# Performance work log

Measured on AMD Instinct MI355X. Metric: run time of the kernel, lower is better.

The kernel has to match this reference:

```python
import jax, jax.numpy as jnp
import numpy as np
import math

B, DG, P, DA = 512, 1024, 1024, 256
LN_EPS = 1e-5  # torch LayerNorm default
EPS = 1e-12


def _ln(x, g, b):
    mu = jnp.mean(x, axis=-1, keepdims=True)
    var = jnp.mean((x - mu) ** 2, axis=-1, keepdims=True)
    return (x - mu) * jax.lax.rsqrt(var + LN_EPS) * g + b


def setup_inputs() -> dict:
    key = jax.random.key(0)
    ks = jax.random.split(key, 16)
    s = lambda fan_in: 1.0 / math.sqrt(fan_in)
    return {
        "hg": jax.random.normal(ks[0], (B, DG), jnp.float32),
        "desc_2d": jax.random.normal(ks[1], (B, P), jnp.float32),
        "Wq": jax.random.uniform(ks[2], (DA, DG), jnp.float32, -s(DG), s(DG)),
        "bq": jnp.zeros((DA,), jnp.float32),
        "wk_val": jax.random.uniform(ks[3], (DA,), jnp.float32, -1.0, 1.0),
        "bk_val": jax.random.uniform(ks[4], (DA,), jnp.float32, -1.0, 1.0),
        "wv_val": jax.random.uniform(ks[5], (DA,), jnp.float32, -1.0, 1.0),
        "bv_val": jax.random.uniform(ks[6], (DA,), jnp.float32, -1.0, 1.0),
        "Ek": jax.random.normal(ks[7], (P, DA), jnp.float32),
        "Ev": jax.random.normal(ks[8], (P, DA), jnp.float32),
        "Uq": jax.random.uniform(ks[9], (DA, DA), jnp.float32, -s(DA), s(DA)),
        "Vk": jax.random.uniform(ks[10], (DA, DA), jnp.float32, -s(DA), s(DA)),
        "ln_q_g": jnp.ones((DA,), jnp.float32), "ln_q_b": jnp.zeros((DA,), jnp.float32),
        "ln_k_g": jnp.ones((DA,), jnp.float32), "ln_k_b": jnp.zeros((DA,), jnp.float32),
        "ln_v_g": jnp.ones((DA,), jnp.float32), "ln_v_b": jnp.zeros((DA,), jnp.float32),
    }


def reference(hg, desc_2d, Wq, bq, wk_val, bk_val, wv_val, bv_val, Ek, Ev, Uq, Vk,
              ln_q_g, ln_q_b, ln_k_g, ln_k_b, ln_v_g, ln_v_b):
    # dropout is inference-mode (identity)
    q = _ln(hg @ Wq.T + bq, ln_q_g, ln_q_b)                       # (B, DA)
    # scalar -> token proj plus id embedding
    k = desc_2d[:, :, None] * wk_val + bk_val + Ek[None]          # (B, P, DA)
    v = desc_2d[:, :, None] * wv_val + bv_val + Ev[None]
    k = _ln(k, ln_k_g, ln_k_b)
    v = _ln(v, ln_v_g, ln_v_b)
    q2 = q @ Uq.T                                                 # (B, DA)
    k2 = jnp.einsum('bpd,ed->bpe', k, Vk)                         # (B, P, DA)
    e = jnp.einsum('bpd,bd->bp', k2, q2) / math.sqrt(DA)          # (B, P)
    alpha = jax.nn.sigmoid(e)
    alpha = alpha / (jnp.sum(alpha, axis=1, keepdims=True) + EPS)
    c = jnp.einsum('bp,bpd->bd', alpha, v)                        # (B, DA)
    return c, alpha
```

## Files before the change

kernel.cpp:

```cpp
#include <hip/hip_runtime.h>
#include <math.h>

#define B 512
#define DG 1024
#define P 1024
#define DA 256
#define LDP 68
#define BP (B * P)
#define BD (B * DA)

__device__ __forceinline__ float block_reduce_sum(float v, volatile float* red) {
    #pragma unroll
    for (int off = 32; off > 0; off >>= 1) v += __shfl_down(v, off, 64);
    const int lane = threadIdx.x & 63, wid = threadIdx.x >> 6;
    __syncthreads();
    if (lane == 0) red[wid] = v;
    __syncthreads();
    return red[0] + red[1] + red[2] + red[3];
}

__device__ __forceinline__ float wsum(float v) {
    #pragma unroll
    for (int m = 32; m > 0; m >>= 1) v += __shfl_xor(v, m, 64);
    return v;
}
__device__ __forceinline__ float txsum(float v) {
    #pragma unroll
    for (int m = 8; m > 0; m >>= 1) v += __shfl_xor(v, m, 16);
    return v;
}

#define FMA16(a4, b4, acc)                                   \
    acc[0][0] = fmaf(a4.x, b4.x, acc[0][0]);                 \
    acc[0][1] = fmaf(a4.x, b4.y, acc[0][1]);                 \
    acc[0][2] = fmaf(a4.x, b4.z, acc[0][2]);                 \
    acc[0][3] = fmaf(a4.x, b4.w, acc[0][3]);                 \
    acc[1][0] = fmaf(a4.y, b4.x, acc[1][0]);                 \
    acc[1][1] = fmaf(a4.y, b4.y, acc[1][1]);                 \
    acc[1][2] = fmaf(a4.y, b4.z, acc[1][2]);                 \
    acc[1][3] = fmaf(a4.y, b4.w, acc[1][3]);                 \
    acc[2][0] = fmaf(a4.z, b4.x, acc[2][0]);                 \
    acc[2][1] = fmaf(a4.z, b4.y, acc[2][1]);                 \
    acc[2][2] = fmaf(a4.z, b4.z, acc[2][2]);                 \
    acc[2][3] = fmaf(a4.z, b4.w, acc[2][3]);                 \
    acc[3][0] = fmaf(a4.w, b4.x, acc[3][0]);                 \
    acc[3][1] = fmaf(a4.w, b4.y, acc[3][1]);                 \
    acc[3][2] = fmaf(a4.w, b4.z, acc[3][2]);                 \
    acc[3][3] = fmaf(a4.w, b4.w, acc[3][3]);

#define FMA8(a0, a1, b4, acc)                                \
    acc[0][0] = fmaf(a0, b4.x, acc[0][0]);                   \
    acc[0][1] = fmaf(a0, b4.y, acc[0][1]);                   \
    acc[0][2] = fmaf(a0, b4.z, acc[0][2]);                   \
    acc[0][3] = fmaf(a0, b4.w, acc[0][3]);                   \
    acc[1][0] = fmaf(a1, b4.x, acc[1][0]);                   \
    acc[1][1] = fmaf(a1, b4.y, acc[1][1]);                   \
    acc[1][2] = fmaf(a1, b4.z, acc[1][2]);                   \
    acc[1][3] = fmaf(a1, b4.w, acc[1][3]);

__device__ __forceinline__ void stage_T(const float* __restrict__ src, int ldk, int m0, int k0,
                                        int tid, float* sD) {
    const int m = tid >> 3, k4 = (tid & 7) * 4;
    #pragma unroll
    for (int pass = 0; pass < 2; ++pass) {
        int mm = m + pass * 32;
        float4 v = *reinterpret_cast<const float4*>(&src[(m0 + mm) * ldk + k0 + k4]);
        sD[(k4 + 0) * LDP + mm] = v.x; sD[(k4 + 1) * LDP + mm] = v.y;
        sD[(k4 + 2) * LDP + mm] = v.z; sD[(k4 + 3) * LDP + mm] = v.w;
    }
}
__device__ __forceinline__ void stage_T32(const float* __restrict__ src, int ldk, int m0, int k0,
                                          int tid, float* sD) {
    const int m = tid >> 3, k4 = (tid & 7) * 4;
    float4 v = *reinterpret_cast<const float4*>(&src[(m0 + m) * ldk + k0 + k4]);
    sD[(k4 + 0) * LDP + m] = v.x; sD[(k4 + 1) * LDP + m] = v.y;
    sD[(k4 + 2) * LDP + m] = v.z; sD[(k4 + 3) * LDP + m] = v.w;
}
__device__ __forceinline__ void stage_N1(const float* __restrict__ src, int ldn, int k0, int n0,
                                         int tid, float* sD) {
    const int k = tid >> 4, n4 = (tid & 15) * 4;
    #pragma unroll
    for (int pass = 0; pass < 2; ++pass) {
        int kk = k + pass * 16;
        *reinterpret_cast<float4*>(&sD[kk * LDP + n4]) =
            *reinterpret_cast<const float4*>(&src[(k0 + kk) * ldn + n0 + n4]);
    }
}
__device__ __forceinline__ void stage_N4(const float* __restrict__ src, int pstride, int ldn,
                                         int k0, int n0, int tid, float* sD) {
    const int k = tid >> 4, n4 = (tid & 15) * 4;
    #pragma unroll
    for (int pass = 0; pass < 2; ++pass) {
        int kk = k + pass * 16;
        const float* base = &src[(k0 + kk) * ldn + n0 + n4];
        float4 v = *reinterpret_cast<const float4*>(base);
        #pragma unroll
        for (int s = 1; s < 4; ++s) {
            float4 w = *reinterpret_cast<const float4*>(base + s * pstride);
            v.x += w.x; v.y += w.y; v.z += w.z; v.w += w.w;
        }
        *reinterpret_cast<float4*>(&sD[kk * LDP + n4]) = v;
    }
}
__device__ __forceinline__ void mm_inner(const float* sA, const float* sB, int tid, float acc[4][4]) {
    const int ty4 = (tid >> 4) * 4, tx4 = (tid & 15) * 4;
    #pragma unroll
    for (int kk = 0; kk < 32; ++kk) {
        float4 a4 = *reinterpret_cast<const float4*>(&sA[kk * LDP + ty4]);
        float4 b4 = *reinterpret_cast<const float4*>(&sB[kk * LDP + tx4]);
        FMA16(a4, b4, acc)
    }
}

__global__ __launch_bounds__(256) void KA(const float* __restrict__ hg, const float* __restrict__ Wq,
                                          const float* __restrict__ Uq, const float* __restrict__ Vk,
                                          const float* __restrict__ Ek, const float* __restrict__ Ev,
                                          const float* __restrict__ wk, const float* __restrict__ bk,
                                          const float* __restrict__ wv, const float* __restrict__ bv,
                                          const float* __restrict__ gk, const float* __restrict__ bkln,
                                          float* __restrict__ qp, float* __restrict__ Gp,
                                          float* __restrict__ UqT, float* __restrict__ Sacc,
                                          float* __restrict__ pst, float* __restrict__ scal4,
                                          float* __restrict__ vec4) {
    __shared__ __align__(16) float sA[32 * LDP];
    __shared__ __align__(16) float sB[32 * LDP];
    const int tid = threadIdx.x;
    const int t = blockIdx.x;
    const int ty4 = (tid >> 4) * 4, tx4 = (tid & 15) * 4;

    if (t < 256) {
        const int mt = t & 7, nt = (t >> 3) & 3, ks = t >> 5;
        const int b0 = mt * 64, d0 = nt * 64, kc = ks * 128;
        float acc[4][4] = {};
        for (int kt = 0; kt < 128; kt += 32) {
            stage_T(hg, DG, b0, kc + kt, tid, sA);
            stage_T(Wq, DG, d0, kc + kt, tid, sB);
            __syncthreads();
            mm_inner(sA, sB, tid, acc);
            __syncthreads();
        }
        float* outp = qp + ks * BD;
        #pragma unroll
        for (int i = 0; i < 4; ++i) {
            float4 o = make_float4(acc[i][0], acc[i][1], acc[i][2], acc[i][3]);
            *reinterpret_cast<float4*>(&outp[(b0 + ty4 + i) * DA + d0 + tx4]) = o;
        }
    } else if (t < 512) {
        const int t2 = t - 256;
        const int et = t2 & 3, pt = (t2 >> 2) & 15, ks = t2 >> 6;
        const int e0 = et * 64, p0 = pt * 64, kc = ks * 64;
        float acc[4][4] = {};
        for (int kt = 0; kt < 64; kt += 32) {
            const int kg = kc + kt;
            {
                const int m = tid >> 3, k4 = (tid & 7) * 4;
                float4 g = *reinterpret_cast<const float4*>(&gk[kg + k4]);
                #pragma unroll
                for (int pass = 0; pass < 2; ++pass) {
                    int mm = m + pass * 32;
                    float4 v = *reinterpret_cast<const float4*>(&Vk[(e0 + mm) * DA + kg + k4]);
                    sA[(k4 + 0) * LDP + mm] = v.x * g.x; sA[(k4 + 1) * LDP + mm] = v.y * g.y;
                    sA[(k4 + 2) * LDP + mm] = v.z * g.z; sA[(k4 + 3) * LDP + mm] = v.w * g.w;
                }
            }
            stage_T(Ek, DA, p0, kg, tid, sB);
            __syncthreads();
            mm_inner(sA, sB, tid, acc);
            __syncthreads();
        }
        float* outp = Gp + ks * (DA * P);
        #pragma unroll
        for (int i = 0; i < 4; ++i) {
            float4 o = make_float4(acc[i][0], acc[i][1], acc[i][2], acc[i][3]);
            *reinterpret_cast<float4*>(&outp[(e0 + ty4 + i) * P + p0 + tx4]) = o;
        }
    } else if (t < 576) {
        const int b2 = t - 512;
        const int e0 = (b2 & 7) * 32, f0 = (b2 >> 3) * 32;
        const int col = tid & 31, row8 = tid >> 5;
        #pragma unroll
        for (int pass = 0; pass < 4; ++pass) {
            int r = row8 + pass * 8;
            sA[r * 33 + col] = Uq[(e0 + r) * DA + f0 + col];
        }
        __syncthreads();
        #pragma unroll
        for (int pass = 0; pass < 4; ++pass) {
            int r = row8 + pass * 8;
            UqT[(f0 + r) * DA + e0 + col] = sA[col * 33 + r];
        }
    } else if (t == 576) {
        #pragma unroll
        for (int j = 0; j < 8; ++j) Sacc[j * 256 + tid] = 0.f;
        float* w4  = sA;
        float* tmp = sB;
        float gkd = gk[tid];
        w4[0 * 256 + tid] = wk[tid] * gkd;
        w4[1 * 256 + tid] = bk[tid] * gkd;
        w4[2 * 256 + tid] = gkd;
        w4[3 * 256 + tid] = bkln[tid];
        __syncthreads();
        const int dl = tid & 15, eg = tid >> 4;
        for (int eb = 0; eb < 16; ++eb) {
            int e = eb * 16 + eg;
            float p0 = 0.f, p1 = 0.f, p2 = 0.f, p3 = 0.f;
            #pragma unroll
            for (int tt = 0; tt < 16; ++tt) {
                int d = dl + tt * 16;
                float v = Vk[e * DA + d];
                p0 = fmaf(v, w4[d], p0);
                p1 = fmaf(v, w4[256 + d], p1);
                p2 = fmaf(v, w4[512 + d], p2);
                p3 = fmaf(v, w4[768 + d], p3);
            }
            #pragma unroll
            for (int m = 8; m > 0; m >>= 1) {
                p0 += __shfl_xor(p0, m, 16);
                p1 += __shfl_xor(p1, m, 16);
                p2 += __shfl_xor(p2, m, 16);
                p3 += __shfl_xor(p3, m, 16);
            }
            if (dl == 0) {
                tmp[e * 4 + 0] = p0; tmp[e * 4 + 1] = p1;
                tmp[e * 4 + 2] = p2; tmp[e * 4 + 3] = p3;
            }
        }
        __syncthreads();
        float a0 = 0.f, a1 = 0.f, a2 = 0.f, a3 = 0.f;
        for (int e = 0; e < 256; ++e) {
            float u = Uq[e * DA + tid];
            a0 = fmaf(u, tmp[e * 4 + 0], a0);
            a1 = fmaf(u, tmp[e * 4 + 1], a1);
            a2 = fmaf(u, tmp[e * 4 + 2], a2);
            a3 = fmaf(u, tmp[e * 4 + 3], a3);
        }
        vec4[tid] = a0; vec4[256 + tid] = a1; vec4[512 + tid] = a2; vec4[768 + tid] = a3;
    } else {
        const int tp = t - 577;
        const int wid = tid >> 6, lane = tid & 63;
        const int p = tp * 4 + wid;
        const int d4 = lane * 4;
        const float inv = 1.0f / DA;
        float4 ek4 = *reinterpret_cast<const float4*>(&Ek[p * DA + d4]);
        float4 ev4 = *reinterpret_cast<const float4*>(&Ev[p * DA + d4]);
        float4 wk4 = *reinterpret_cast<const float4*>(&wk[d4]);
        float4 bk4 = *reinterpret_cast<const float4*>(&bk[d4]);
        float4 wv4 = *reinterpret_cast<const float4*>(&wv[d4]);
        float4 bv4 = *reinterpret_cast<const float4*>(&bv[d4]);
        float ck0 = bk4.x + ek4.x, ck1 = bk4.y + ek4.y, ck2 = bk4.z + ek4.z, ck3 = bk4.w + ek4.w;
        float cv0 = bv4.x + ev4.x, cv1 = bv4.y + ev4.y, cv2 = bv4.z + ev4.z, cv3 = bv4.w + ev4.w;
        float Sck  = wsum(ck0 + ck1 + ck2 + ck3);
        float Sck2 = wsum(ck0*ck0 + ck1*ck1 + ck2*ck2 + ck3*ck3);
        float Swck = wsum(wk4.x*ck0 + wk4.y*ck1 + wk4.z*ck2 + wk4.w*ck3);
        float Scv  = wsum(cv0 + cv1 + cv2 + cv3);
        float Scv2 = wsum(cv0*cv0 + cv1*cv1 + cv2*cv2 + cv3*cv3);
        float Swcv = wsum(wv4.x*cv0 + wv4.y*cv1 + wv4.z*cv2 + wv4.w*cv3);
        float Swk  = wsum(wk4.x + wk4.y + wk4.z + wk4.w);
        float Swv  = wsum(wv4.x + wv4.y + wv4.z + wv4.w);
        float mwk = Swk * inv, mwv = Swv * inv;
        float mck = Sck * inv, mcv = Scv * inv;
        if (lane == 0) {
            pst[0 * P + p] = mck;
            pst[1 * P + p] = Swck * inv - mwk * mck;
            pst[2 * P + p] = Sck2 * inv - mck * mck;
            pst[3 * P + p] = mcv;
            pst[4 * P + p] = Swcv * inv - mwv * mcv;
            pst[5 * P + p] = Scv2 * inv - mcv * mcv;
        }
        if (p == 0) {
            float Swk2 = wsum(wk4.x*wk4.x + wk4.y*wk4.y + wk4.z*wk4.z + wk4.w*wk4.w);
            float Swv2 = wsum(wv4.x*wv4.x + wv4.y*wv4.y + wv4.z*wv4.z + wv4.w*wv4.w);
            if (lane == 0) {
                scal4[0] = mwk;
                scal4[1] = Swk2 * inv - mwk * mwk;
                scal4[2] = mwv;
                scal4[3] = Swv2 * inv - mwv * mwv;
            }
        }
    }
}

__global__ __launch_bounds__(256) void KC(const float* __restrict__ qp, const float* __restrict__ bq,
                                          const float* __restrict__ gq, const float* __restrict__ bqln,
                                          const float* __restrict__ vec4, const float* __restrict__ UqT,
                                          float* __restrict__ q2out, float* __restrict__ bscal) {
    __shared__ __align__(16) float q_lds[DA];
    __shared__ float red[4];
    const int b = blockIdx.x, d = threadIdx.x;
    float x = bq[d];
    #pragma unroll
    for (int ks = 0; ks < 8; ++ks) x += qp[ks * BD + b * DA + d];
    float mu = block_reduce_sum(x, red) * (1.0f / DA);
    float xc = x - mu;
    float var = block_reduce_sum(xc * xc, red) * (1.0f / DA);
    float qv = xc * rsqrtf(var + 1e-5f) * gq[d] + bqln[d];
    q_lds[d] = qv;
    float Wg = block_reduce_sum(qv * vec4[d], red);
    float Cg = block_reduce_sum(qv * vec4[256 + d], red);
    float G_ = block_reduce_sum(qv * vec4[512 + d], red);
    float Bb = block_reduce_sum(qv * vec4[768 + d], red);
    if (d == 0) {
        bscal[b] = Wg; bscal[B + b] = Cg;
        bscal[2 * B + b] = G_; bscal[3 * B + b] = Bb;
    }
    float q2 = 0.f;
    for (int f = 0; f < DA; f += 4) {
        float4 qf = *reinterpret_cast<const float4*>(&q_lds[f]);
        q2 = fmaf(qf.x, UqT[(f + 0) * DA + d], q2);
        q2 = fmaf(qf.y, UqT[(f + 1) * DA + d], q2);
        q2 = fmaf(qf.z, UqT[(f + 2) * DA + d], q2);
        q2 = fmaf(qf.w, UqT[(f + 3) * DA + d], q2);
    }
    q2out[b * DA + d] = q2;
}

__global__ __launch_bounds__(256) void KD(const float* __restrict__ q2, const float* __restrict__ Gp,
                                          const float* __restrict__ desc, const float* __restrict__ bscal,
                                          const float* __restrict__ pst, const float* __restrict__ scal4,
                                          float* __restrict__ ubuf, float* __restrict__ wbuf,
                                          float* __restrict__ Sacc) {
    __shared__ __align__(16) float sA[32 * LDP];
    __shared__ __align__(16) float sB[32 * LDP];
    const int tid = threadIdx.x, t = blockIdx.x;
    const int tx = tid & 15, ty = tid >> 4;
    const int tx4 = tx * 4;
    const int b0 = (t & 15) * 32, p0 = (t >> 4) * 64;
    float acc[2][4] = {};
    for (int kt = 0; kt < 256; kt += 32) {
        stage_T32(q2, DA, b0, kt, tid, sA);
        stage_N4(Gp, DA * P, P, kt, p0, tid, sB);
        __syncthreads();
        #pragma unroll
        for (int kk = 0; kk < 32; ++kk) {
            float a0 = sA[kk * LDP + ty * 2 + 0];
            float a1 = sA[kk * LDP + ty * 2 + 1];
            float4 b4 = *reinterpret_cast<const float4*>(&sB[kk * LDP + tx4]);
            FMA8(a0, a1, b4, acc)
        }
        __syncthreads();
    }
    const float mwk = scal4[0], Ak = scal4[1], mwv = scal4[2], Av = scal4[3];
    #pragma unroll
    for (int i = 0; i < 2; ++i) {
        const int b = b0 + ty * 2 + i;
        const float Wg = bscal[b], Cg = bscal[B + b], G_ = bscal[2 * B + b], Bb = bscal[3 * B + b];
        float4 uo, wo;
        float* up = &uo.x; float* wp = &wo.x;
        float us = 0.f, ws_ = 0.f, wss = 0.f, wms = 0.f;
        #pragma unroll
        for (int j = 0; j < 4; ++j) {
            const int p = p0 + tx4 + j;
            float s = desc[b * P + p];
            float mck = pst[p], Bk = pst[P + p], Ck = pst[2 * P + p];
            float var = fmaf(s, fmaf(s, Ak, 2.0f * Bk), Ck);
            float rstd = rsqrtf(var + 1e-5f);
            float mu = fmaf(s, mwk, mck);
            float e = (rstd * (fmaf(s, Wg, Cg) + acc[i][j] - mu * G_) + Bb) * 0.0625f;
            float uu = 1.0f / (1.0f + expf(-e));
            float mcv = pst[3 * P + p], Bv = pst[4 * P + p], Cv = pst[5 * P + p];
            float varv = fmaf(s, fmaf(s, Av, 2.0f * Bv), Cv);
            float rv = rsqrtf(varv + 1e-5f);
            float ww = uu * rv;
            up[j] = uu; wp[j] = ww;
            us += uu; ws_ += ww;
            wss = fmaf(ww, s, wss);
            wms = fmaf(ww, fmaf(s, mwv, mcv), wms);
        }
        *reinterpret_cast<float4*>(&ubuf[b * P + p0 + tx4]) = uo;
        *reinterpret_cast<float4*>(&wbuf[b * P + p0 + tx4]) = wo;
        us = txsum(us); ws_ = txsum(ws_); wss = txsum(wss); wms = txsum(wms);
        if (tx == 0) {
            atomicAdd(&Sacc[b], us);
            atomicAdd(&Sacc[B + b], ws_);
            atomicAdd(&Sacc[2 * B + b], wss);
            atomicAdd(&Sacc[3 * B + b], wms);
        }
    }
}

__global__ __launch_bounds__(256) void KF(const float* __restrict__ wbuf, const float* __restrict__ Ev,
                                          float* __restrict__ cpart) {
    __shared__ __align__(16) float sA[32 * LDP];
    __shared__ __align__(16) float sB[32 * LDP];
    const int tid = threadIdx.x, t = blockIdx.x;
    const int ty4 = (tid >> 4) * 4, tx4 = (tid & 15) * 4;
    const int mt = t & 7, nt = (t >> 3) & 3, ks = t >> 5;
    const int b0 = mt * 64, d0 = nt * 64, kc = ks * 128;
    float acc[4][4] = {};
    for (int kt = 0; kt < 128; kt += 32) {
        stage_T(wbuf, P, b0, kc + kt, tid, sA);
        stage_N1(Ev, DA, kc + kt, d0, tid, sB);
        __syncthreads();
        mm_inner(sA, sB, tid, acc);
        __syncthreads();
    }
    float* outp = cpart + ks * BD;
    #pragma unroll
    for (int i = 0; i < 4; ++i) {
        float4 o = make_float4(acc[i][0], acc[i][1], acc[i][2], acc[i][3]);
        *reinterpret_cast<float4*>(&outp[(b0 + ty4 + i) * DA + d0 + tx4]) = o;
    }
}

__global__ __launch_bounds__(256) void KG(const float* __restrict__ cpart, const float* __restrict__ Sacc,
                                          const float* __restrict__ ubuf,
                                          const float* __restrict__ gv, const float* __restrict__ wv,
                                          const float* __restrict__ bvv, const float* __restrict__ bvln,
                                          float* __restrict__ alpha_out, float* __restrict__ out_c) {
    const int b = blockIdx.x, tid = threadIdx.x;
    const float S = Sacc[b], SB = Sacc[B + b], SBs = Sacc[2 * B + b], SBm = Sacc[3 * B + b];
    const float invS = 1.0f / (S + 1e-12f);
    const float T = S * invS;
    #pragma unroll
    for (int j = 0; j < 4; ++j) {
        int p = j * 256 + tid;
        alpha_out[b * P + p] = ubuf[b * P + p] * invS;
    }
    const int d = tid;
    float csum = 0.f;
    #pragma unroll
    for (int ks = 0; ks < 8; ++ks) csum += cpart[ks * BD + b * DA + d];
    out_c[b * DA + d] =
        invS * (gv[d] * (wv[d] * SBs + bvv[d] * SB + csum - SBm)) + bvln[d] * T;
}

extern "C" void kernel_launch(void* const* d_in, const int* in_sizes, int n_in,
                              void* d_out, int out_size, void* d_ws, size_t ws_size,
                              hipStream_t stream) {
    (void)in_sizes; (void)n_in; (void)out_size; (void)ws_size;
    const float* hg   = (const float*)d_in[0];
    const float* desc = (const float*)d_in[1];
    const float* Wq   = (const float*)d_in[2];
    const float* bq   = (const float*)d_in[3];
    const float* wk   = (const float*)d_in[4];
    const float* bk   = (const float*)d_in[5];
    const float* wv   = (const float*)d_in[6];
    const float* bv   = (const float*)d_in[7];
    const float* Ek   = (const float*)d_in[8];
    const float* Ev   = (const float*)d_in[9];
    const float* Uq   = (const float*)d_in[10];
    const float* Vk   = (const float*)d_in[11];
    const float* gq   = (const float*)d_in[12];
    const float* bqln = (const float*)d_in[13];
    const float* gk   = (const float*)d_in[14];
    const float* bkln = (const float*)d_in[15];
    const float* gv   = (const float*)d_in[16];
    const float* bvln = (const float*)d_in[17];

    float* out = (float*)d_out;
    float* out_c = out;
    float* out_alpha = out + BD;

    float* ws = (float*)d_ws;
    float* qp    = ws;
    float* Gp    = ws + 1048576;
    float* UqT   = ws + 2097152;
    float* q2    = ws + 2162688;
    float* ubuf  = ws + 2293760;
    float* wbuf  = ws + 2818048;
    float* cpart = ws + 3342336;
    float* vec4  = ws + 4390912;
    float* bscal = ws + 4391936;
    float* Sacc  = ws + 4393984;
    float* pst   = ws + 4396032;
    float* scal4 = ws + 4402176;

    KA<<<833, 256, 0, stream>>>(hg, Wq, Uq, Vk, Ek, Ev, wk, bk, wv, bv, gk, bkln,
                                qp, Gp, UqT, Sacc, pst, scal4, vec4);
    KC<<<512, 256, 0, stream>>>(qp, bq, gq, bqln, vec4, UqT, q2, bscal);
    KD<<<256, 256, 0, stream>>>(q2, Gp, desc, bscal, pst, scal4, ubuf, wbuf, Sacc);
    KF<<<256, 256, 0, stream>>>(wbuf, Ev, cpart);
    KG<<<512, 256, 0, stream>>>(cpart, Sacc, ubuf, gv, wv, bv, bvln, out_alpha, out_c);
}
```

Baseline: 70.31 us.

## Fuse five kernels into one persistent kernel with grid-wide atomic barriers

Replaces the five separate kernel launches with one persistent 256-block kernel. Each former kernel becomes a phase that loops over its tiles, and phases are separated by a software grid barrier built on atomic counters that a memset clears before launch. The Vk·Ek split-K factor also drops from 4 to 2 partials, so the score stage sums fewer slices of Gp. This removes launch gaps and the tail between kernels, but it depends on all 256 blocks being co-resident. It also has to run many phases with fewer blocks than the original grids (833 and 512 tiles).

```diff
diff --git a/kernel.cpp b/kernel.cpp
--- a/kernel.cpp
+++ b/kernel.cpp
@@ -8,6 +8,7 @@
 #define LDP 68
 #define BP (B * P)
 #define BD (B * DA)
+#define NBLK 256
 
 __device__ __forceinline__ float block_reduce_sum(float v, volatile float* red) {
     #pragma unroll
@@ -18,7 +19,6 @@
     __syncthreads();
     return red[0] + red[1] + red[2] + red[3];
 }
-
 __device__ __forceinline__ float wsum(float v) {
     #pragma unroll
     for (int m = 32; m > 0; m >>= 1) v += __shfl_xor(v, m, 64);
@@ -86,7 +86,7 @@
             *reinterpret_cast<const float4*>(&src[(k0 + kk) * ldn + n0 + n4]);
     }
 }
-__device__ __forceinline__ void stage_N4(const float* __restrict__ src, int pstride, int ldn,
+__device__ __forceinline__ void stage_N2(const float* __restrict__ src, int pstride, int ldn,
                                          int k0, int n0, int tid, float* sD) {
     const int k = tid >> 4, n4 = (tid & 15) * 4;
     #pragma unroll
@@ -94,11 +94,8 @@
         int kk = k + pass * 16;
         const float* base = &src[(k0 + kk) * ldn + n0 + n4];
         float4 v = *reinterpret_cast<const float4*>(base);
-        #pragma unroll
-        for (int s = 1; s < 4; ++s) {
-            float4 w = *reinterpret_cast<const float4*>(base + s * pstride);
-            v.x += w.x; v.y += w.y; v.z += w.z; v.w += w.w;
-        }
+        float4 w = *reinterpret_cast<const float4*>(base + pstride);
+        v.x += w.x; v.y += w.y; v.z += w.z; v.w += w.w;
         *reinterpret_cast<float4*>(&sD[kk * LDP + n4]) = v;
     }
 }
@@ -112,363 +109,360 @@
     }
 }
 
-__global__ __launch_bounds__(256) void KA(const float* __restrict__ hg, const float* __restrict__ Wq,
-                                          const float* __restrict__ Uq, const float* __restrict__ Vk,
-                                          const float* __restrict__ Ek, const float* __restrict__ Ev,
-                                          const float* __restrict__ wk, const float* __restrict__ bk,
-                                          const float* __restrict__ wv, const float* __restrict__ bv,
-                                          const float* __restrict__ gk, const float* __restrict__ bkln,
-                                          float* __restrict__ qp, float* __restrict__ Gp,
-                                          float* __restrict__ UqT, float* __restrict__ Sacc,
-                                          float* __restrict__ pst, float* __restrict__ scal4,
-                                          float* __restrict__ vec4) {
+__device__ __forceinline__ void gbar(unsigned* cnt, int ph) {
+    __syncthreads();
+    if (threadIdx.x == 0) {
+        __threadfence();
+        atomicAdd(&cnt[ph], 1u);
+        while (atomicAdd(&cnt[ph], 0u) < (unsigned)NBLK) {
+            __builtin_amdgcn_s_sleep(2);
+        }
+        __threadfence();
+    }
+    __syncthreads();
+}
+
+struct KArgs {
+    const float *hg, *desc, *Wq, *bq, *wk, *bk, *wv, *bv, *Ek, *Ev, *Uq, *Vk;
+    const float *gq, *bqln, *gk, *bkln, *gv, *bvln;
+    float *out_c, *out_alpha;
+    float *Sacc; unsigned* cnt;
+    float *qp, *Gp, *UqT, *q2, *ubuf, *wbuf, *cpart, *vec4, *bscal, *pst, *scal4;
+};
+
+__global__ __launch_bounds__(256) void mega(KArgs A) {
     __shared__ __align__(16) float sA[32 * LDP];
     __shared__ __align__(16) float sB[32 * LDP];
-    const int tid = threadIdx.x;
-    const int t = blockIdx.x;
+    __shared__ float red[4];
+    const int tid = threadIdx.x, bid = blockIdx.x;
     const int ty4 = (tid >> 4) * 4, tx4 = (tid & 15) * 4;
 
-    if (t < 256) {
+    for (int t = bid; t < 705; t += NBLK) {
+        if (t < 256) {
+            const int mt = t & 7, nt = (t >> 3) & 3, ks = t >> 5;
+            const int b0 = mt * 64, d0 = nt * 64, kc = ks * 128;
+            float acc[4][4] = {};
+            for (int kt = 0; kt < 128; kt += 32) {
+                stage_T(A.hg, DG, b0, kc + kt, tid, sA);
+                stage_T(A.Wq, DG, d0, kc + kt, tid, sB);
+                __syncthreads();
+                mm_inner(sA, sB, tid, acc);
+                __syncthreads();
+            }
+            float* outp = A.qp + ks * BD;
+            #pragma unroll
+            for (int i = 0; i < 4; ++i) {
+                float4 o = make_float4(acc[i][0], acc[i][1], acc[i][2], acc[i][3]);
+                *reinterpret_cast<float4*>(&outp[(b0 + ty4 + i) * DA + d0 + tx4]) = o;
+            }
+        } else if (t < 384) {
+            const int t2 = t - 256;
+            const int et = t2 & 3, pt = (t2 >> 2) & 15, ks = t2 >> 6;
+            const int e0 = et * 64, p0 = pt * 64, kc = ks * 128;
+            float acc[4][4] = {};
+            for (int kt = 0; kt < 128; kt += 32) {
+                const int kg = kc + kt;
+                {
+                    const int m = tid >> 3, k4 = (tid & 7) * 4;
+                    float4 g = *reinterpret_cast<const float4*>(&A.gk[kg + k4]);
+                    #pragma unroll
+                    for (int pass = 0; pass < 2; ++pass) {
+                        int mm = m + pass * 32;
+                        float4 v = *reinterpret_cast<const float4*>(&A.Vk[(e0 + mm) * DA + kg + k4]);
+                        sA[(k4 + 0) * LDP + mm] = v.x * g.x; sA[(k4 + 1) * LDP + mm] = v.y * g.y;
+                        sA[(k4 + 2) * LDP + mm] = v.z * g.z; sA[(k4 + 3) * LDP + mm] = v.w * g.w;
+                    }
+                }
+                stage_T(A.Ek, DA, p0, kg, tid, sB);
+                __syncthreads();
+                mm_inner(sA, sB, tid, acc);
+                __syncthreads();
+            }
+            float* outp = A.Gp + ks * (DA * P);
+            #pragma unroll
+            for (int i = 0; i < 4; ++i) {
+                float4 o = make_float4(acc[i][0], acc[i][1], acc[i][2], acc[i][3]);
+                *reinterpret_cast<float4*>(&outp[(e0 + ty4 + i) * P + p0 + tx4]) = o;
+            }
+        } else if (t < 448) {
+            const int b2 = t - 384;
+            const int e0 = (b2 & 7) * 32, f0 = (b2 >> 3) * 32;
+            const int col = tid & 31, row8 = tid >> 5;
+            #pragma unroll
+            for (int pass = 0; pass < 4; ++pass) {
+                int r = row8 + pass * 8;
+                sA[r * 33 + col] = A.Uq[(e0 + r) * DA + f0 + col];
+            }
+            __syncthreads();
+            #pragma unroll
+            for (int pass = 0; pass < 4; ++pass) {
+                int r = row8 + pass * 8;
+                A.UqT[(f0 + r) * DA + e0 + col] = sA[col * 33 + r];
+            }
+        } else if (t == 448) {
+            float* w4  = sA;
+            float* tmp = sB;
+            float gkd = A.gk[tid];
+            w4[0 * 256 + tid] = A.wk[tid] * gkd;
+            w4[1 * 256 + tid] = A.bk[tid] * gkd;
+            w4[2 * 256 + tid] = gkd;
+            w4[3 * 256 + tid] = A.bkln[tid];
+            __syncthreads();
+            const int dl = tid & 15, eg = tid >> 4;
+            for (int eb = 0; eb < 16; ++eb) {
+                int e = eb * 16 + eg;
+                float p0 = 0.f, p1 = 0.f, p2 = 0.f, p3 = 0.f;
+                #pragma unroll
+                for (int tt = 0; tt < 16; ++tt) {
+                    int d = dl + tt * 16;
+                    float v = A.Vk[e * DA + d];
+                    p0 = fmaf(v, w4[d], p0);
+                    p1 = fmaf(v, w4[256 + d], p1);
+                    p2 = fmaf(v, w4[512 + d], p2);
+                    p3 = fmaf(v, w4[768 + d], p3);
+                }
+                #pragma unroll
+                for (int m = 8; m > 0; m >>= 1) {
+                    p0 += __shfl_xor(p0, m, 16);
+                    p1 += __shfl_xor(p1, m, 16);
+                    p2 += __shfl_xor(p2, m, 16);
+                    p3 += __shfl_xor(p3, m, 16);
+                }
+                if (dl == 0) {
+                    tmp[e * 4 + 0] = p0; tmp[e * 4 + 1] = p1;
+                    tmp[e * 4 + 2] = p2; tmp[e * 4 + 3] = p3;
+                }
+            }
+            __syncthreads();
+            float a0 = 0.f, a1 = 0.f, a2 = 0.f, a3 = 0.f;
+            for (int e = 0; e < 256; ++e) {
+                float u = A.Uq[e * DA + tid];
+                a0 = fmaf(u, tmp[e * 4 + 0], a0);
+                a1 = fmaf(u, tmp[e * 4 + 1], a1);
+                a2 = fmaf(u, tmp[e * 4 + 2], a2);
+                a3 = fmaf(u, tmp[e * 4 + 3], a3);
+            }
+            A.vec4[tid] = a0; A.vec4[256 + tid] = a1;
+            A.vec4[512 + tid] = a2; A.vec4[768 + tid] = a3;
+        } else {
+            const int tp = t - 449;
+            const int wid = tid >> 6, lane = tid & 63;
+            const int p = tp * 4 + wid;
+            const int d4 = lane * 4;
+            const float inv = 1.0f / DA;
+            float4 ek4 = *reinterpret_cast<const float4*>(&A.Ek[p * DA + d4]);
+            float4 ev4 = *reinterpret_cast<const float4*>(&A.Ev[p * DA + d4]);
+            float4 wk4 = *reinterpret_cast<const float4*>(&A.wk[d4]);
+            float4 bk4 = *reinterpret_cast<const float4*>(&A.bk[d4]);
+            float4 wv4 = *reinterpret_cast<const float4*>(&A.wv[d4]);
+            float4 bv4 = *reinterpret_cast<const float4*>(&A.bv[d4]);
+            float ck0 = bk4.x + ek4.x, ck1 = bk4.y + ek4.y, ck2 = bk4.z + ek4.z, ck3 = bk4.w + ek4.w;
+            float cv0 = bv4.x + ev4.x, cv1 = bv4.y + ev4.y, cv2 = bv4.z + ev4.z, cv3 = bv4.w + ev4.w;
+            float Sck  = wsum(ck0 + ck1 + ck2 + ck3);
+            float Sck2 = wsum(ck0*ck0 + ck1*ck1 + ck2*ck2 + ck3*ck3);
+            float Swck = wsum(wk4.x*ck0 + wk4.y*ck1 + wk4.z*ck2 + wk4.w*ck3);
+            float Scv  = wsum(cv0 + cv1 + cv2 + cv3);
+            float Scv2 = wsum(cv0*cv0 + cv1*cv1 + cv2*cv2 + cv3*cv3);
+            float Swcv = wsum(wv4.x*cv0 + wv4.y*cv1 + wv4.z*cv2 + wv4.w*cv3);
+            float Swk  = wsum(wk4.x + wk4.y + wk4.z + wk4.w);
+            float Swv  = wsum(wv4.x + wv4.y + wv4.z + wv4.w);
+            float mwk = Swk * inv, mwv = Swv * inv;
+            float mck = Sck * inv, mcv = Scv * inv;
+            if (lane == 0) {
+                A.pst[0 * P + p] = mck;
+                A.pst[1 * P + p] = Swck * inv - mwk * mck;
+                A.pst[2 * P + p] = Sck2 * inv - mck * mck;
+                A.pst[3 * P + p] = mcv;
+                A.pst[4 * P + p] = Swcv * inv - mwv * mcv;
+                A.pst[5 * P + p] = Scv2 * inv - mcv * mcv;
+            }
+            if (p == 0) {
+                float Swk2 = wsum(wk4.x*wk4.x + wk4.y*wk4.y + wk4.z*wk4.z + wk4.w*wk4.w);
+                float Swv2 = wsum(wv4.x*wv4.x + wv4.y*wv4.y + wv4.z*wv4.z + wv4.w*wv4.w);
+                if (lane == 0) {
+                    A.scal4[0] = mwk;
+                    A.scal4[1] = Swk2 * inv - mwk * mwk;
+                    A.scal4[2] = mwv;
+                    A.scal4[3] = Swv2 * inv - mwv * mwv;
+                }
+            }
+        }
+        __syncthreads();
+    }
+    gbar(A.cnt, 0);
+
+    for (int t = bid; t < 512; t += NBLK) {
+        const int b = t, d = tid;
+        float* q_lds = sA;
+        float x = A.bq[d];
+        #pragma unroll
+        for (int ks = 0; ks < 8; ++ks) x += A.qp[ks * BD + b * DA + d];
+        float mu = block_reduce_sum(x, red) * (1.0f / DA);
+        float xc = x - mu;
+        float var = block_reduce_sum(xc * xc, red) * (1.0f / DA);
+        float qv = xc * rsqrtf(var + 1e-5f) * A.gq[d] + A.bqln[d];
+        q_lds[d] = qv;
+        float Wg = block_reduce_sum(qv * A.vec4[d], red);
+        float Cg = block_reduce_sum(qv * A.vec4[256 + d], red);
+        float G_ = block_reduce_sum(qv * A.vec4[512 + d], red);
+        float Bb = block_reduce_sum(qv * A.vec4[768 + d], red);
+        if (d == 0) {
+            A.bscal[b] = Wg; A.bscal[B + b] = Cg;
+            A.bscal[2 * B + b] = G_; A.bscal[3 * B + b] = Bb;
+        }
+        float q2 = 0.f;
+        for (int f = 0; f < DA; f += 4) {
+            float4 qf = *reinterpret_cast<const float4*>(&q_lds[f]);
+            q2 = fmaf(qf.x, A.UqT[(f + 0) * DA + d], q2);
+            q2 = fmaf(qf.y, A.UqT[(f + 1) * DA + d], q2);
+            q2 = fmaf(qf.z, A.UqT[(f + 2) * DA + d], q2);
+            q2 = fmaf(qf.w, A.UqT[(f + 3) * DA + d], q2);
+        }
+        A.q2[b * DA + d] = q2;
+        __syncthreads();
+    }
+    gbar(A.cnt, 1);
+
+    for (int t = bid; t < 256; t += NBLK) {
+        const int tx = tid & 15, ty = tid >> 4;
+        const int b0 = (t & 15) * 32, p0 = (t >> 4) * 64;
+        float acc[2][4] = {};
+        for (int kt = 0; kt < 256; kt += 32) {
+            stage_T32(A.q2, DA, b0, kt, tid, sA);
+            stage_N2(A.Gp, DA * P, P, kt, p0, tid, sB);
+            __syncthreads();
+            #pragma unroll
+            for (int kk = 0; kk < 32; ++kk) {
+                float a0 = sA[kk * LDP + ty * 2 + 0];
+                float a1 = sA[kk * LDP + ty * 2 + 1];
+                float4 b4 = *reinterpret_cast<const float4*>(&sB[kk * LDP + tx4]);
+                FMA8(a0, a1, b4, acc)
+            }
+            __syncthreads();
+        }
+        const float mwk = A.scal4[0], Ak = A.scal4[1], mwv = A.scal4[2], Av = A.scal4[3];
+        #pragma unroll
+        for (int i = 0; i < 2; ++i) {
+            const int b = b0 + ty * 2 + i;
+            const float Wg = A.bscal[b], Cg = A.bscal[B + b];
+            const float G_ = A.bscal[2 * B + b], Bb = A.bscal[3 * B + b];
+            float4 uo, wo;
+            float* up = &uo.x; float* wp = &wo.x;
+            float us = 0.f, ws_ = 0.f, wss = 0.f, wms = 0.f;
+            #pragma unroll
+            for (int j = 0; j < 4; ++j) {
+                const int p = p0 + tx4 + j;
+                float s = A.desc[b * P + p];
+                float mck = A.pst[p], Bk = A.pst[P + p], Ck = A.pst[2 * P + p];
+                float var = fmaf(s, fmaf(s, Ak, 2.0f * Bk), Ck);
+                float rstd = rsqrtf(var + 1e-5f);
+                float mu = fmaf(s, mwk, mck);
+                float e = (rstd * (fmaf(s, Wg, Cg) + acc[i][j] - mu * G_) + Bb) * 0.0625f;
+                float uu = 1.0f / (1.0f + expf(-e));
+                float mcv = A.pst[3 * P + p], Bv = A.pst[4 * P + p], Cv = A.pst[5 * P + p];
+                float varv = fmaf(s, fmaf(s, Av, 2.0f * Bv), Cv);
+                float rv = rsqrtf(varv + 1e-5f);
+                float ww = uu * rv;
+                up[j] = uu; wp[j] = ww;
+                us += uu; ws_ += ww;
+                wss = fmaf(ww, s, wss);
+                wms = fmaf(ww, fmaf(s, mwv, mcv), wms);
+            }
+            *reinterpret_cast<float4*>(&A.ubuf[b * P + p0 + tx4]) = uo;
+            *reinterpret_cast<float4*>(&A.wbuf[b * P + p0 + tx4]) = wo;
+            us = txsum(us); ws_ = txsum(ws_); wss = txsum(wss); wms = txsum(wms);
+            if (tx == 0) {
+                atomicAdd(&A.Sacc[b], us);
+                atomicAdd(&A.Sacc[B + b], ws_);
+                atomicAdd(&A.Sacc[2 * B + b], wss);
+                atomicAdd(&A.Sacc[3 * B + b], wms);
+            }
+        }
+        __syncthreads();
+    }
+    gbar(A.cnt, 2);
+
+    for (int t = bid; t < 256; t += NBLK) {
         const int mt = t & 7, nt = (t >> 3) & 3, ks = t >> 5;
         const int b0 = mt * 64, d0 = nt * 64, kc = ks * 128;
         float acc[4][4] = {};
         for (int kt = 0; kt < 128; kt += 32) {
-            stage_T(hg, DG, b0, kc + kt, tid, sA);
-            stage_T(Wq, DG, d0, kc + kt, tid, sB);
+            stage_T(A.wbuf, P, b0, kc + kt, tid, sA);
+            stage_N1(A.Ev, DA, kc + kt, d0, tid, sB);
             __syncthreads();
             mm_inner(sA, sB, tid, acc);
             __syncthreads();
         }
-        float* outp = qp + ks * BD;
+        float* outp = A.cpart + ks * BD;
         #pragma unroll
         for (int i = 0; i < 4; ++i) {
             float4 o = make_float4(acc[i][0], acc[i][1], acc[i][2], acc[i][3]);
             *reinterpret_cast<float4*>(&outp[(b0 + ty4 + i) * DA + d0 + tx4]) = o;
         }
-    } else if (t < 512) {
-        const int t2 = t - 256;
-        const int et = t2 & 3, pt = (t2 >> 2) & 15, ks = t2 >> 6;
-        const int e0 = et * 64, p0 = pt * 64, kc = ks * 64;
-        float acc[4][4] = {};
-        for (int kt = 0; kt < 64; kt += 32) {
-            const int kg = kc + kt;
-            {
-                const int m = tid >> 3, k4 = (tid & 7) * 4;
-                float4 g = *reinterpret_cast<const float4*>(&gk[kg + k4]);
-                #pragma unroll
-                for (int pass = 0; pass < 2; ++pass) {
-                    int mm = m + pass * 32;
-                    float4 v = *reinterpret_cast<const float4*>(&Vk[(e0 + mm) * DA + kg + k4]);
-                    sA[(k4 + 0) * LDP + mm] = v.x * g.x; sA[(k4 + 1) * LDP + mm] = v.y * g.y;
-                    sA[(k4 + 2) * LDP + mm] = v.z * g.z; sA[(k4 + 3) * LDP + mm] = v.w * g.w;
-                }
-            }
-            stage_T(Ek, DA, p0, kg, tid, sB);
-            __syncthreads();
-            mm_inner(sA, sB, tid, acc);
-            __syncthreads();
-        }
-        float* outp = Gp + ks * (DA * P);
-        #pragma unroll
-        for (int i = 0; i < 4; ++i) {
-            float4 o = make_float4(acc[i][0], acc[i][1], acc[i][2], acc[i][3]);
-            *reinterpret_cast<float4*>(&outp[(e0 + ty4 + i) * P + p0 + tx4]) = o;
-        }
-    } else if (t < 576) {
-        const int b2 = t - 512;
-        const int e0 = (b2 & 7) * 32, f0 = (b2 >> 3) * 32;
-        const int col = tid & 31, row8 = tid >> 5;
-        #pragma unroll
-        for (int pass = 0; pass < 4; ++pass) {
-            int r = row8 + pass * 8;
-            sA[r * 33 + col] = Uq[(e0 + r) * DA + f0 + col];
-        }
         __syncthreads();
-        #pragma unroll
-        for (int pass = 0; pass < 4; ++pass) {
-            int r = row8 + pass * 8;
-            UqT[(f0 + r) * DA + e0 + col] = sA[col * 33 + r];
-        }
-    } else if (t == 576) {
-        #pragma unroll
-        for (int j = 0; j < 8; ++j) Sacc[j * 256 + tid] = 0.f;
-        float* w4  = sA;
-        float* tmp = sB;
-        float gkd = gk[tid];
-        w4[0 * 256 + tid] = wk[tid] * gkd;
-        w4[1 * 256 + tid] = bk[tid] * gkd;
-        w4[2 * 256 + tid] = gkd;
-        w4[3 * 256 + tid] = bkln[tid];
-        __syncthreads();
-        const int dl = tid & 15, eg = tid >> 4;
-        for (int eb = 0; eb < 16; ++eb) {
-            int e = eb * 16 + eg;
-            float p0 = 0.f, p1 = 0.f, p2 = 0.f, p3 = 0.f;
-            #pragma unroll
-            for (int tt = 0; tt < 16; ++tt) {
-                int d = dl + tt * 16;
-                float v = Vk[e * DA + d];
-                p0 = fmaf(v, w4[d], p0);
-                p1 = fmaf(v, w4[256 + d], p1);
-                p2 = fmaf(v, w4[512 + d], p2);
-                p3 = fmaf(v, w4[768 + d], p3);
-            }
-            #pragma unroll
-            for (int m = 8; m > 0; m >>= 1) {
-                p0 += __shfl_xor(p0, m, 16);
-                p1 += __shfl_xor(p1, m, 16);
-                p2 += __shfl_xor(p2, m, 16);
-                p3 += __shfl_xor(p3, m, 16);
-            }
-            if (dl == 0) {
-                tmp[e * 4 + 0] = p0; tmp[e * 4 + 1] = p1;
-                tmp[e * 4 + 2] = p2; tmp[e * 4 + 3] = p3;
-            }
-        }
-        __syncthreads();
-        float a0 = 0.f, a1 = 0.f, a2 = 0.f, a3 = 0.f;
-        for (int e = 0; e < 256; ++e) {
-            float u = Uq[e * DA + tid];
-            a0 = fmaf(u, tmp[e * 4 + 0], a0);
-            a1 = fmaf(u, tmp[e * 4 + 1], a1);
-            a2 = fmaf(u, tmp[e * 4 + 2], a2);
-            a3 = fmaf(u, tmp[e * 4 + 3], a3);
-        }
-        vec4[tid] = a0; vec4[256 + tid] = a1; vec4[512 + tid] = a2; vec4[768 + tid] = a3;
-    } else {
-        const int tp = t - 577;
-        const int wid = tid >> 6, lane = tid & 63;
-        const int p = tp * 4 + wid;
-        const int d4 = lane * 4;
-        const float inv = 1.0f / DA;
-        float4 ek4 = *reinterpret_cast<const float4*>(&Ek[p * DA + d4]);
-        float4 ev4 = *reinterpret_cast<const float4*>(&Ev[p * DA + d4]);
-        float4 wk4 = *reinterpret_cast<const float4*>(&wk[d4]);
-        float4 bk4 = *reinterpret_cast<const float4*>(&bk[d4]);
-        float4 wv4 = *reinterpret_cast<const float4*>(&wv[d4]);
-        float4 bv4 = *reinterpret_cast<const float4*>(&bv[d4]);
-        float ck0 = bk4.x + ek4.x, ck1 = bk4.y + ek4.y, ck2 = bk4.z + ek4.z, ck3 = bk4.w + ek4.w;
-        float cv0 = bv4.x + ev4.x, cv1 = bv4.y + ev4.y, cv2 = bv4.z + ev4.z, cv3 = bv4.w + ev4.w;
-        float Sck  = wsum(ck0 + ck1 + ck2 + ck3);
-        float Sck2 = wsum(ck0*ck0 + ck1*ck1 + ck2*ck2 + ck3*ck3);
-        float Swck = wsum(wk4.x*ck0 + wk4.y*ck1 + wk4.z*ck2 + wk4.w*ck3);
-        float Scv  = wsum(cv0 + cv1 + cv2 + cv3);
-        float Scv2 = wsum(cv0*cv0 + cv1*cv1 + cv2*cv2 + cv3*cv3);
-        float Swcv = wsum(wv4.x*cv0 + wv4.y*cv1 + wv4.z*cv2 + wv4.w*cv3);
-        float Swk  = wsum(wk4.x + wk4.y + wk4.z + wk4.w);
-        float Swv  = wsum(wv4.x + wv4.y + wv4.z + wv4.w);
-        float mwk = Swk * inv, mwv = Swv * inv;
-        float mck = Sck * inv, mcv = Scv * inv;
-        if (lane == 0) {
-            pst[0 * P + p] = mck;
-            pst[1 * P + p] = Swck * inv - mwk * mck;
-            pst[2 * P + p] = Sck2 * inv - mck * mck;
-            pst[3 * P + p] = mcv;
-            pst[4 * P + p] = Swcv * inv - mwv * mcv;
-            pst[5 * P + p] = Scv2 * inv - mcv * mcv;
-        }
-        if (p == 0) {
-            float Swk2 = wsum(wk4.x*wk4.x + wk4.y*wk4.y + wk4.z*wk4.z + wk4.w*wk4.w);
-            float Swv2 = wsum(wv4.x*wv4.x + wv4.y*wv4.y + wv4.z*wv4.z + wv4.w*wv4.w);
-            if (lane == 0) {
-                scal4[0] = mwk;
-                scal4[1] = Swk2 * inv - mwk * mwk;
-                scal4[2] = mwv;
-                scal4[3] = Swv2 * inv - mwv * mwv;
-            }
-        }
-    }
-}
-
-__global__ __launch_bounds__(256) void KC(const float* __restrict__ qp, const float* __restrict__ bq,
-                                          const float* __restrict__ gq, const float* __restrict__ bqln,
-                                          const float* __restrict__ vec4, const float* __restrict__ UqT,
-                                          float* __restrict__ q2out, float* __restrict__ bscal) {
-    __shared__ __align__(16) float q_lds[DA];
-    __shared__ float red[4];
-    const int b = blockIdx.x, d = threadIdx.x;
-    float x = bq[d];
-    #pragma unroll
-    for (int ks = 0; ks < 8; ++ks) x += qp[ks * BD + b * DA + d];
-    float mu = block_reduce_sum(x, red) * (1.0f / DA);
-    float xc = x - mu;
-    float var = block_reduce_sum(xc * xc, red) * (1.0f / DA);
-    float qv = xc * rsqrtf(var + 1e-5f) * gq[d] + bqln[d];
-    q_lds[d] = qv;
-    float Wg = block_reduce_sum(qv * vec4[d], red);
-    float Cg = block_reduce_sum(qv * vec4[256 + d], red);
-    float G_ = block_reduce_sum(qv * vec4[512 + d], red);
-    float Bb = block_reduce_sum(qv * vec4[768 + d], red);
-    if (d == 0) {
-        bscal[b] = Wg; bscal[B + b] = Cg;
-        bscal[2 * B + b] = G_; bscal[3 * B + b] = Bb;
-    }
-    float q2 = 0.f;
-    for (int f = 0; f < DA; f += 4) {
-        float4 qf = *reinterpret_cast<const float4*>(&q_lds[f]);
-        q2 = fmaf(qf.x, UqT[(f + 0) * DA + d], q2);
-        q2 = fmaf(qf.y, UqT[(f + 1) * DA + d], q2);
-        q2 = fmaf(qf.z, UqT[(f + 2) * DA + d], q2);
-        q2 = fmaf(qf.w, UqT[(f + 3) * DA + d], q2);
-    }
-    q2out[b * DA + d] = q2;
-}
-
-__global__ __launch_bounds__(256) void KD(const float* __restrict__ q2, const float* __restrict__ Gp,
-                                          const float* __restrict__ desc, const float* __restrict__ bscal,
-                                          const float* __restrict__ pst, const float* __restrict__ scal4,
-                                          float* __restrict__ ubuf, float* __restrict__ wbuf,
-                                          float* __restrict__ Sacc) {
-    __shared__ __align__(16) float sA[32 * LDP];
-    __shared__ __align__(16) float sB[32 * LDP];
-    const int tid = threadIdx.x, t = blockIdx.x;
-    const int tx = tid & 15, ty = tid >> 4;
-    const int tx4 = tx * 4;
-    const int b0 = (t & 15) * 32, p0 = (t >> 4) * 64;
-    float acc[2][4] = {};
-    for (int kt = 0; kt < 256; kt += 32) {
-        stage_T32(q2, DA, b0, kt, tid, sA);
-        stage_N4(Gp, DA * P, P, kt, p0, tid, sB);
-        __syncthreads();
-        #pragma unroll
-        for (int kk = 0; kk < 32; ++kk) {
-            float a0 = sA[kk * LDP + ty * 2 + 0];
-            float a1 = sA[kk * LDP + ty * 2 + 1];
-            float4 b4 = *reinterpret_cast<const float4*>(&sB[kk * LDP + tx4]);
-            FMA8(a0, a1, b4, acc)
-        }
-        __syncthreads();
-    }
-    const float mwk = scal4[0], Ak = scal4[1], mwv = scal4[2], Av = scal4[3];
-    #pragma unroll
-    for (int i = 0; i < 2; ++i) {
-        const int b = b0 + ty * 2 + i;
-        const float Wg = bscal[b], Cg = bscal[B + b], G_ = bscal[2 * B + b], Bb = bscal[3 * B + b];
-        float4 uo, wo;
-        float* up = &uo.x; float* wp = &wo.x;
-        float us = 0.f, ws_ = 0.f, wss = 0.f, wms = 0.f;
+    }
+    gbar(A.cnt, 3);
+
+    for (int t = bid; t < 512; t += NBLK) {
+        const int b = t, d = tid;
+        const float S = A.Sacc[b], SB = A.Sacc[B + b];
+        const float SBs = A.Sacc[2 * B + b], SBm = A.Sacc[3 * B + b];
+        const float invS = 1.0f / (S + 1e-12f);
+        const float T = S * invS;
         #pragma unroll
         for (int j = 0; j < 4; ++j) {
-            const int p = p0 + tx4 + j;
-            float s = desc[b * P + p];
-            float mck = pst[p], Bk = pst[P + p], Ck = pst[2 * P + p];
-            float var = fmaf(s, fmaf(s, Ak, 2.0f * Bk), Ck);
-            float rstd = rsqrtf(var + 1e-5f);
-            float mu = fmaf(s, mwk, mck);
-            float e = (rstd * (fmaf(s, Wg, Cg) + acc[i][j] - mu * G_) + Bb) * 0.0625f;
-            float uu = 1.0f / (1.0f + expf(-e));
-            float mcv = pst[3 * P + p], Bv = pst[4 * P + p], Cv = pst[5 * P + p];
-            float varv = fmaf(s, fmaf(s, Av, 2.0f * Bv), Cv);
-            float rv = rsqrtf(varv + 1e-5f);
-            float ww = uu * rv;
-            up[j] = uu; wp[j] = ww;
-            us += uu; ws_ += ww;
-            wss = fmaf(ww, s, wss);
-            wms = fmaf(ww, fmaf(s, mwv, mcv), wms);
-        }
-        *reinterpret_cast<float4*>(&ubuf[b * P + p0 + tx4]) = uo;
-        *reinterpret_cast<float4*>(&wbuf[b * P + p0 + tx4]) = wo;
-        us = txsum(us); ws_ = txsum(ws_); wss = txsum(wss); wms = txsum(wms);
-        if (tx == 0) {
-            atomicAdd(&Sacc[b], us);
-            atomicAdd(&Sacc[B + b], ws_);
-            atomicAdd(&Sacc[2 * B + b], wss);
-            atomicAdd(&Sacc[3 * B + b], wms);
-        }
-    }
-}
-
-__global__ __launch_bounds__(256) void KF(const float* __restrict__ wbuf, const float* __restrict__ Ev,
-                                          float* __restrict__ cpart) {
-    __shared__ __align__(16) float sA[32 * LDP];
-    __shared__ __align__(16) float sB[32 * LDP];
-    const int tid = threadIdx.x, t = blockIdx.x;
-    const int ty4 = (tid >> 4) * 4, tx4 = (tid & 15) * 4;
-    const int mt = t & 7, nt = (t >> 3) & 3, ks = t >> 5;
-    const int b0 = mt * 64, d0 = nt * 64, kc = ks * 128;
-    float acc[4][4] = {};
-    for (int kt = 0; kt < 128; kt += 32) {
-        stage_T(wbuf, P, b0, kc + kt, tid, sA);
-        stage_N1(Ev, DA, kc + kt, d0, tid, sB);
-        __syncthreads();
-        mm_inner(sA, sB, tid, acc);
-        __syncthreads();
-    }
-    float* outp = cpart + ks * BD;
-    #pragma unroll
-    for (int i = 0; i < 4; ++i) {
-        float4 o = make_float4(acc[i][0], acc[i][1], acc[i][2], acc[i][3]);
-        *reinterpret_cast<float4*>(&outp[(b0 + ty4 + i) * DA + d0 + tx4]) = o;
-    }
-}
-
-__global__ __launch_bounds__(256) void KG(const float* __restrict__ cpart, const float* __restrict__ Sacc,
-                                          const float* __restrict__ ubuf,
-                                          const float* __restrict__ gv, const float* __restrict__ wv,
-                                          const float* __restrict__ bvv, const float* __restrict__ bvln,
-                                          float* __restrict__ alpha_out, float* __restrict__ out_c) {
-    const int b = blockIdx.x, tid = threadIdx.x;
-    const float S = Sacc[b], SB = Sacc[B + b], SBs = Sacc[2 * B + b], SBm = Sacc[3 * B + b];
-    const float invS = 1.0f / (S + 1e-12f);
-    const float T = S * invS;
-    #pragma unroll
-    for (int j = 0; j < 4; ++j) {
-        int p = j * 256 + tid;
-        alpha_out[b * P + p] = ubuf[b * P + p] * invS;
-    }
-    const int d = tid;
-    float csum = 0.f;
-    #pragma unroll
-    for (int ks = 0; ks < 8; ++ks) csum += cpart[ks * BD + b * DA + d];
-    out_c[b * DA + d] =
-        invS * (gv[d] * (wv[d] * SBs + bvv[d] * SB + csum - SBm)) + bvln[d] * T;
+            int p = j * 256 + d;
+            A.out_alpha[b * P + p] = A.ubuf[b * P + p] * invS;
+        }
+        float csum = 0.f;
+        #pragma unroll
+        for (int ks = 0; ks < 8; ++ks) csum += A.cpart[ks * BD + b * DA + d];
+        A.out_c[b * DA + d] =
+            invS * (A.gv[d] * (A.wv[d] * SBs + A.bv[d] * SB + csum - SBm)) + A.bvln[d] * T;
+    }
 }
 
 extern "C" void kernel_launch(void* const* d_in, const int* in_sizes, int n_in,
                               void* d_out, int out_size, void* d_ws, size_t ws_size,
                               hipStream_t stream) {
     (void)in_sizes; (void)n_in; (void)out_size; (void)ws_size;
-    const float* hg   = (const float*)d_in[0];
-    const float* desc = (const float*)d_in[1];
-    const float* Wq   = (const float*)d_in[2];
-    const float* bq   = (const float*)d_in[3];
-    const float* wk   = (const float*)d_in[4];
-    const float* bk   = (const float*)d_in[5];
-    const float* wv   = (const float*)d_in[6];
-    const float* bv   = (const float*)d_in[7];
-    const float* Ek   = (const float*)d_in[8];
-    const float* Ev   = (const float*)d_in[9];
-    const float* Uq   = (const float*)d_in[10];
-    const float* Vk   = (const float*)d_in[11];
-    const float* gq   = (const float*)d_in[12];
-    const float* bqln = (const float*)d_in[13];
-    const float* gk   = (const float*)d_in[14];
-    const float* bkln = (const float*)d_in[15];
-    const float* gv   = (const float*)d_in[16];
-    const float* bvln = (const float*)d_in[17];
-
-    float* out = (float*)d_out;
-    float* out_c = out;
-    float* out_alpha = out + BD;
-
     float* ws = (float*)d_ws;
-    float* qp    = ws;
-    float* Gp    = ws + 1048576;
-    float* UqT   = ws + 2097152;
-    float* q2    = ws + 2162688;
-    float* ubuf  = ws + 2293760;
-    float* wbuf  = ws + 2818048;
-    float* cpart = ws + 3342336;
-    float* vec4  = ws + 4390912;
-    float* bscal = ws + 4391936;
-    float* Sacc  = ws + 4393984;
-    float* pst   = ws + 4396032;
-    float* scal4 = ws + 4402176;
-
-    KA<<<833, 256, 0, stream>>>(hg, Wq, Uq, Vk, Ek, Ev, wk, bk, wv, bv, gk, bkln,
-                                qp, Gp, UqT, Sacc, pst, scal4, vec4);
-    KC<<<512, 256, 0, stream>>>(qp, bq, gq, bqln, vec4, UqT, q2, bscal);
-    KD<<<256, 256, 0, stream>>>(q2, Gp, desc, bscal, pst, scal4, ubuf, wbuf, Sacc);
-    KF<<<256, 256, 0, stream>>>(wbuf, Ev, cpart);
-    KG<<<512, 256, 0, stream>>>(cpart, Sacc, ubuf, gv, wv, bv, bvln, out_alpha, out_c);
-}
+    KArgs a;
+    a.hg   = (const float*)d_in[0];
+    a.desc = (const float*)d_in[1];
+    a.Wq   = (const float*)d_in[2];
+    a.bq   = (const float*)d_in[3];
+    a.wk   = (const float*)d_in[4];
+    a.bk   = (const float*)d_in[5];
+    a.wv   = (const float*)d_in[6];
+    a.bv   = (const float*)d_in[7];
+    a.Ek   = (const float*)d_in[8];
+    a.Ev   = (const float*)d_in[9];
+    a.Uq   = (const float*)d_in[10];
+    a.Vk   = (const float*)d_in[11];
+    a.gq   = (const float*)d_in[12];
+    a.bqln = (const float*)d_in[13];
+    a.gk   = (const float*)d_in[14];
+    a.bkln = (const float*)d_in[15];
+    a.gv   = (const float*)d_in[16];
+    a.bvln = (const float*)d_in[17];
+    a.out_c     = (float*)d_out;
+    a.out_alpha = (float*)d_out + BD;
+
+    a.Sacc  = ws;
+    a.cnt   = (unsigned*)(ws + 2048);
+    a.qp    = ws + 4096;
+    a.Gp    = ws + 1052672;
+    a.UqT   = ws + 1576960;
+    a.q2    = ws + 1642496;
+    a.ubuf  = ws + 1773568;
+    a.wbuf  = ws + 2297856;
+    a.cpart = ws + 2822144;
+    a.vec4  = ws + 3870720;
+    a.bscal = ws + 3871744;
+    a.pst   = ws + 3873792;
+    a.scal4 = ws + 3879936;
+
+    hipMemsetAsync(d_ws, 0, 8448, stream);
+    mega<<<NBLK, 256, 0, stream>>>(a);
+}
```

Result: slower. 160.4 us (+128.1%).
